# Kernel tuning notes

Measured on AMD Instinct MI355X. Metric: run time of the kernel, lower is better.

Reference implementation:

```python
import jax, jax.numpy as jnp
import numpy as np

EPS = 1e-5  # BatchNorm eps


def cbr(x, W, g, b, m, v):
    # 1x1 Conv (no bias) + inference BatchNorm + ReLU
    # x: [B,Cin,H,W], W: [Cout,Cin]
    y = jnp.einsum('oc,bchw->bohw', W, x)
    inv = g / jnp.sqrt(v + EPS)            # [Cout]
    y = y * inv[None, :, None, None] + (b - m * inv)[None, :, None, None]
    return jax.nn.relu(y)


def setup_inputs() -> dict:
    key = jax.random.key(0)
    ks = jax.random.split(key, 32)
    B, C, R, H, W = 4, 2048, 512, 64, 64
    d = {"feature": jax.random.normal(ks[0], (B, C, H, W), jnp.float32)}
    idx = 1
    for name, (cin, cout) in [("r", (C, R)), ("q", (R, R)), ("k", (R, R)), ("v", (R, R)), ("u", (R, C))]:
        d[name + "_W"] = jax.random.normal(ks[idx], (cout, cin), jnp.float32) * 0.02
        d[name + "_g"] = jax.random.uniform(ks[idx + 1], (cout,), jnp.float32)
        d[name + "_b"] = jax.random.normal(ks[idx + 2], (cout,), jnp.float32) * 0.1
        d[name + "_m"] = jax.random.normal(ks[idx + 3], (cout,), jnp.float32) * 0.1
        d[name + "_v"] = jax.random.uniform(ks[idx + 4], (cout,), jnp.float32)
        idx += 5
    return d


def reference(feature, r_W, r_g, r_b, r_m, r_v,
              q_W, q_g, q_b, q_m, q_v,
              k_W, k_g, k_b, k_m, k_v,
              v_W, v_g, v_b, v_m, v_v,
              u_W, u_g, u_b, u_m, u_v):
    B, C, H, W = feature.shape
    f = cbr(feature, r_W, r_g, r_b, r_m, r_v)          # [B,R,H,W]
    R = f.shape[1]
    N = H * W
    q = cbr(f, q_W, q_g, q_b, q_m, q_v).reshape(B, R, N)
    k = cbr(f, k_W, k_g, k_b, k_m, k_v).reshape(B, R, N)
    v = cbr(f, v_W, v_g, v_b, v_m, v_v).reshape(B, R, N)
    # similarity map over all spatial positions: [B,N,N]
    attn = jax.nn.softmax(jnp.einsum('bcn,bcm->bnm', q, k), axis=-1)
    upd = jnp.einsum('bnm,bcm->bnc', attn, v)          # [B,N,R]
    upd = upd.reshape(B, H, W, R).transpose(0, 3, 1, 2)  # [B,R,H,W]
    return cbr(f + upd, u_W, u_g, u_b, u_m, u_v)       # [B,C,H,W]
```

## Files before the change

kernel.cpp:

```cpp
#include <hip/hip_runtime.h>

#define EPSV 1e-5f

typedef unsigned short u16;
typedef __attribute__((ext_vector_type(8))) _Float16 half8;
typedef __attribute__((ext_vector_type(4))) float floatx4;

__device__ __forceinline__ float h2f(u16 h) {
    return (float)__builtin_bit_cast(_Float16, h);
}
__device__ __forceinline__ u16 f2h(float f) {
    _Float16 h = (_Float16)f;
    return __builtin_bit_cast(u16, h);
}

template <int MODE, typename OUTT>
__global__ __launch_bounds__(256)
void gemm_nt(const u16* __restrict__ A, const u16* __restrict__ B,
             OUTT* __restrict__ C_,
             const float* __restrict__ inv_, const float* __restrict__ beta_,
             const u16* __restrict__ addf,
             int K, int ldA, int ldB, int ldC,
             long strideA, long strideB, long strideC)
{
    __shared__ u16 As[128 * 32];
    __shared__ u16 Bs[128 * 32];

    const int tid = threadIdx.x;
    const int w = tid >> 6;
    const int l = tid & 63;
    const int j0 = blockIdx.x * 128;
    const int i0 = blockIdx.y * 128;

    const u16* Ab = A + (long)blockIdx.z * strideA;
    const u16* Bb = B + (long)blockIdx.z * strideB;

    const int srow = w * 16 + (l >> 2);
    const int skel = (l & 3) * 8;

    const int i_base = (w >> 1) * 64;
    const int j_base = (w & 1) * 64;
    const int lm = l & 15;
    const int kq = l >> 4;

    floatx4 acc[4][4];
    #pragma unroll
    for (int a = 0; a < 4; ++a)
        #pragma unroll
        for (int b = 0; b < 4; ++b) acc[a][b] = (floatx4)(0.0f);

    for (int k0 = 0; k0 < K; k0 += 32) {
        const u16* ga0 = Ab + (long)(i0 + srow) * ldA + k0 + skel;
        const u16* ga1 = Ab + (long)(i0 + 64 + srow) * ldA + k0 + skel;
        const u16* gb0 = Bb + (long)(j0 + srow) * ldB + k0 + skel;
        const u16* gb1 = Bb + (long)(j0 + 64 + srow) * ldB + k0 + skel;
        char* la0 = (char*)As + w * 1024;
        char* la1 = (char*)As + 4096 + w * 1024;
        char* lb0 = (char*)Bs + w * 1024;
        char* lb1 = (char*)Bs + 4096 + w * 1024;
        __builtin_amdgcn_global_load_lds(
            (const __attribute__((address_space(1))) unsigned int*)(const void*)ga0,
            (__attribute__((address_space(3))) unsigned int*)(void*)la0, 16, 0, 0);
        __builtin_amdgcn_global_load_lds(
            (const __attribute__((address_space(1))) unsigned int*)(const void*)ga1,
            (__attribute__((address_space(3))) unsigned int*)(void*)la1, 16, 0, 0);
        __builtin_amdgcn_global_load_lds(
            (const __attribute__((address_space(1))) unsigned int*)(const void*)gb0,
            (__attribute__((address_space(3))) unsigned int*)(void*)lb0, 16, 0, 0);
        __builtin_amdgcn_global_load_lds(
            (const __attribute__((address_space(1))) unsigned int*)(const void*)gb1,
            (__attribute__((address_space(3))) unsigned int*)(void*)lb1, 16, 0, 0);
        __syncthreads();

        half8 af[4], bf[4];
        #pragma unroll
        for (int t = 0; t < 4; ++t) {
            af[t] = *(const half8*)&As[(i_base + t * 16 + lm) * 32 + kq * 8];
            bf[t] = *(const half8*)&Bs[(j_base + t * 16 + lm) * 32 + kq * 8];
        }
        #pragma unroll
        for (int ti = 0; ti < 4; ++ti)
            #pragma unroll
            for (int tj = 0; tj < 4; ++tj)
                acc[ti][tj] = __builtin_amdgcn_mfma_f32_16x16x32_f16(
                    af[ti], bf[tj], acc[ti][tj], 0, 0, 0);
        __syncthreads();
    }

    OUTT* Cb = C_ + (long)blockIdx.z * strideC;
    const u16* addb = (MODE == 3) ? addf + (long)blockIdx.z * strideC : nullptr;
    #pragma unroll
    for (int ti = 0; ti < 4; ++ti) {
        #pragma unroll
        for (int tj = 0; tj < 4; ++tj) {
            const int jj = j0 + j_base + tj * 16 + lm;
            float cinv = 0.f, cbeta = 0.f;
            if (MODE == 1) { cinv = inv_[jj]; cbeta = beta_[jj]; }
            #pragma unroll
            for (int r = 0; r < 4; ++r) {
                const int ii = i0 + i_base + ti * 16 + kq * 4 + r;
                float val = acc[ti][tj][r];
                if (MODE == 1) val = fmaxf(val * cinv + cbeta, 0.0f);
                if (MODE == 2) {
                    float iv = inv_[ii], bt = beta_[ii];
                    val = fmaxf(val * iv + bt, 0.0f);
                }
                if (MODE == 3) val += h2f(addb[(long)ii * ldC + jj]);
                if (sizeof(OUTT) == 4) {
                    ((float*)Cb)[(long)ii * ldC + jj] = val;
                } else {
                    ((u16*)Cb)[(long)ii * ldC + jj] = f2h(val);
                }
            }
        }
    }
}

__global__ __launch_bounds__(256)
void conv_weight(const float* __restrict__ W, const float* __restrict__ g,
                 const float* __restrict__ b, const float* __restrict__ m,
                 const float* __restrict__ v,
                 u16* __restrict__ Wb, float* __restrict__ inv_,
                 float* __restrict__ beta_, int cout, long n)
{
    for (long idx = (long)blockIdx.x * 256 + threadIdx.x; idx < n;
         idx += (long)gridDim.x * 256)
        Wb[idx] = f2h(W[idx]);
    int c = blockIdx.x * 256 + threadIdx.x;
    if (c < cout) {
        float iv = g[c] * rsqrtf(v[c] + EPSV);
        inv_[c] = iv;
        beta_[c] = b[c] - m[c] * iv;
    }
}

__global__ __launch_bounds__(256)
void transpose_conv(const float* __restrict__ in, u16* __restrict__ out,
                    int C, int N)
{
    __shared__ float t[32][33];
    const int n0 = blockIdx.x * 32, c0 = blockIdx.y * 32;
    const float* inb = in + (long)blockIdx.z * C * N;
    u16* outb = out + (long)blockIdx.z * C * N;
    const int tx = threadIdx.x & 31, ty = threadIdx.x >> 5;
    #pragma unroll
    for (int rr = 0; rr < 32; rr += 8)
        t[ty + rr][tx] = inb[(long)(c0 + ty + rr) * N + n0 + tx];
    __syncthreads();
    #pragma unroll
    for (int rr = 0; rr < 32; rr += 8)
        outb[(long)(n0 + ty + rr) * C + c0 + tx] = f2h(t[tx][ty + rr]);
}

__global__ __launch_bounds__(256)
void softmax_f16(const float* __restrict__ S, u16* __restrict__ P)
{
    __shared__ float buf[4096];
    __shared__ float red[256];
    const float* p = S + (long)blockIdx.y * 4096 * 4096 + (long)blockIdx.x * 4096;
    u16* o = P + (long)blockIdx.y * 4096 * 4096 + (long)blockIdx.x * 4096;
    const int tid = threadIdx.x;

    float lmax = -3.4e38f;
    for (int i = tid; i < 4096; i += 256) {
        float x = p[i];
        buf[i] = x;
        lmax = fmaxf(lmax, x);
    }
    red[tid] = lmax;
    __syncthreads();
    for (int s = 128; s > 0; s >>= 1) {
        if (tid < s) red[tid] = fmaxf(red[tid], red[tid + s]);
        __syncthreads();
    }
    const float mx = red[0];
    __syncthreads();

    float lsum = 0.0f;
    for (int i = tid; i < 4096; i += 256) {
        float e = __expf(buf[i] - mx);
        buf[i] = e;
        lsum += e;
    }
    red[tid] = lsum;
    __syncthreads();
    for (int s = 128; s > 0; s >>= 1) {
        if (tid < s) red[tid] += red[tid + s];
        __syncthreads();
    }
    const float invs = 1.0f / red[0];
    __syncthreads();

    for (int i = tid; i < 4096; i += 256) o[i] = f2h(buf[i] * invs);
}

extern "C" void kernel_launch(void* const* d_in, const int* in_sizes, int n_in,
                              void* d_out, int out_size, void* d_ws, size_t ws_size,
                              hipStream_t stream)
{
    (void)in_sizes; (void)n_in; (void)out_size; (void)ws_size;
    constexpr int B = 4, C = 2048, R = 512, N = 4096;
    constexpr long NR = (long)N * R;
    constexpr long NC = (long)N * C;
    constexpr long NN = (long)N * N;

    const float* feature = (const float*)d_in[0];
    const float* W_[5]  = {(const float*)d_in[1],  (const float*)d_in[6],
                           (const float*)d_in[11], (const float*)d_in[16],
                           (const float*)d_in[21]};
    const float* G_[5]  = {(const float*)d_in[2],  (const float*)d_in[7],
                           (const float*)d_in[12], (const float*)d_in[17],
                           (const float*)d_in[22]};
    const float* Bb_[5] = {(const float*)d_in[3],  (const float*)d_in[8],
                           (const float*)d_in[13], (const float*)d_in[18],
                           (const float*)d_in[23]};
    const float* M_[5]  = {(const float*)d_in[4],  (const float*)d_in[9],
                           (const float*)d_in[14], (const float*)d_in[19],
                           (const float*)d_in[24]};
    const float* V_[5]  = {(const float*)d_in[5],  (const float*)d_in[10],
                           (const float*)d_in[15], (const float*)d_in[20],
                           (const float*)d_in[25]};
    const int cout_[5] = {R, R, R, R, C};
    const int cin_[5]  = {C, R, R, R, R};

    char* base = (char*)d_ws;
    size_t off = 0;
    float* S     = (float*)base;
    u16*   featT = (u16*)base;
    off += (size_t)B * NN * 4;
    u16* fT = (u16*)(base + off);                      off += (size_t)B * NR * 2;
    u16* qT = (u16*)(base + off);                      off += (size_t)B * NR * 2;
    u16* kT = (u16*)(base + off);                      off += (size_t)B * NR * 2;
    u16* vC = (u16*)(base + off);                      off += (size_t)B * NR * 2;
    u16* gT = (u16*)(base + off);                      off += (size_t)B * NR * 2;
    u16* Pc = (u16*)(base + off);                      off += (size_t)B * NN * 2;
    u16* Wb_[5]; float* inv_[5]; float* beta_[5];
    for (int i = 0; i < 5; ++i) {
        Wb_[i] = (u16*)(base + off);  off += (size_t)cout_[i] * cin_[i] * 2;
        off = (off + 255) & ~(size_t)255;
    }
    for (int i = 0; i < 5; ++i) {
        inv_[i]  = (float*)(base + off);  off += 8192;
        beta_[i] = (float*)(base + off);  off += 8192;
    }

    float* out = (float*)d_out;
    const dim3 blk(256);

    for (int i = 0; i < 5; ++i)
        conv_weight<<<512, blk, 0, stream>>>(W_[i], G_[i], Bb_[i], M_[i], V_[i],
                                             Wb_[i], inv_[i], beta_[i],
                                             cout_[i], (long)cout_[i] * cin_[i]);

    transpose_conv<<<dim3(N / 32, C / 32, B), blk, 0, stream>>>(feature, featT, C, N);

    gemm_nt<1, u16><<<dim3(R / 128, N / 128, B), blk, 0, stream>>>(
        featT, Wb_[0], fT, inv_[0], beta_[0], nullptr,
        C, C, C, R, NC, 0, NR);

    gemm_nt<1, u16><<<dim3(R / 128, N / 128, B), blk, 0, stream>>>(
        fT, Wb_[1], qT, inv_[1], beta_[1], nullptr,
        R, R, R, R, NR, 0, NR);
    gemm_nt<1, u16><<<dim3(R / 128, N / 128, B), blk, 0, stream>>>(
        fT, Wb_[2], kT, inv_[2], beta_[2], nullptr,
        R, R, R, R, NR, 0, NR);
    gemm_nt<2, u16><<<dim3(N / 128, R / 128, B), blk, 0, stream>>>(
        Wb_[3], fT, vC, inv_[3], beta_[3], nullptr,
        R, R, R, N, 0, NR, NR);

    gemm_nt<0, float><<<dim3(N / 128, N / 128, B), blk, 0, stream>>>(
        qT, kT, S, nullptr, nullptr, nullptr,
        R, R, R, N, NR, NR, NN);

    softmax_f16<<<dim3(N, B), blk, 0, stream>>>(S, Pc);

    gemm_nt<3, u16><<<dim3(R / 128, N / 128, B), blk, 0, stream>>>(
        Pc, vC, gT, nullptr, nullptr, fT,
        N, N, N, R, NN, NR, NR);

    gemm_nt<2, float><<<dim3(N / 128, C / 128, B), blk, 0, stream>>>(
        Wb_[4], gT, out, inv_[4], beta_[4], nullptr,
        R, R, R, N, 0, NR, NC);
}
```

Before: 828.5 us.

## Double-buffer GEMM LDS tiles, swizzle workgroup order, fuse Q/K projections

The GEMM kernel now uses two LDS buffers and issues global-to-LDS loads for the next K-slice before computing on the current one, so memory latency can overlap with MFMA work. Workgroup IDs are remapped with a stride-8 swizzle, likely to spread consecutive blocks across XCDs and improve cache locality. The Q and K projection GEMMs are merged into one GEMM with concatenated weights that writes an interleaved qk buffer, and the QK^T GEMM reads it with stride 1024. Doubling LDS per block may lower occupancy. There is also only one barrier per iteration while the next stage writes the buffer that was read in the previous iteration, which relies on that barrier for ordering.

```diff
diff --git a/kernel.cpp b/kernel.cpp
--- a/kernel.cpp
+++ b/kernel.cpp
@@ -23,17 +23,31 @@
              int K, int ldA, int ldB, int ldC,
              long strideA, long strideB, long strideC)
 {
-    __shared__ u16 As[128 * 32];
-    __shared__ u16 Bs[128 * 32];
+    __shared__ u16 As[2][128 * 32];
+    __shared__ u16 Bs[2][128 * 32];
 
     const int tid = threadIdx.x;
     const int w = tid >> 6;
     const int l = tid & 63;
-    const int j0 = blockIdx.x * 128;
-    const int i0 = blockIdx.y * 128;
-
-    const u16* Ab = A + (long)blockIdx.z * strideA;
-    const u16* Bb = B + (long)blockIdx.z * strideB;
+
+    int bx = blockIdx.x, by = blockIdx.y, bz = blockIdx.z;
+    {
+        const int gx = gridDim.x, gy = gridDim.y;
+        const int nwg = gx * gy * (int)gridDim.z;
+        if ((nwg & 7) == 0) {
+            const int lin = bx + gx * (by + gy * bz);
+            const int swz = (lin & 7) * (nwg >> 3) + (lin >> 3);
+            bx = swz % gx;
+            const int t = swz / gx;
+            by = t % gy;
+            bz = t / gy;
+        }
+    }
+    const int j0 = bx * 128;
+    const int i0 = by * 128;
+
+    const u16* Ab = A + (long)bz * strideA;
+    const u16* Bb = B + (long)bz * strideB;
 
     const int srow = w * 16 + (l >> 2);
     const int skel = (l & 3) * 8;
@@ -49,15 +63,15 @@
         #pragma unroll
         for (int b = 0; b < 4; ++b) acc[a][b] = (floatx4)(0.0f);
 
-    for (int k0 = 0; k0 < K; k0 += 32) {
+    auto stage = [&](int buf, int k0) {
         const u16* ga0 = Ab + (long)(i0 + srow) * ldA + k0 + skel;
         const u16* ga1 = Ab + (long)(i0 + 64 + srow) * ldA + k0 + skel;
         const u16* gb0 = Bb + (long)(j0 + srow) * ldB + k0 + skel;
         const u16* gb1 = Bb + (long)(j0 + 64 + srow) * ldB + k0 + skel;
-        char* la0 = (char*)As + w * 1024;
-        char* la1 = (char*)As + 4096 + w * 1024;
-        char* lb0 = (char*)Bs + w * 1024;
-        char* lb1 = (char*)Bs + 4096 + w * 1024;
+        char* la0 = (char*)&As[buf][0] + w * 1024;
+        char* la1 = (char*)&As[buf][0] + 4096 + w * 1024;
+        char* lb0 = (char*)&Bs[buf][0] + w * 1024;
+        char* lb1 = (char*)&Bs[buf][0] + 4096 + w * 1024;
         __builtin_amdgcn_global_load_lds(
             (const __attribute__((address_space(1))) unsigned int*)(const void*)ga0,
             (__attribute__((address_space(3))) unsigned int*)(void*)la0, 16, 0, 0);
@@ -70,13 +84,20 @@
         __builtin_amdgcn_global_load_lds(
             (const __attribute__((address_space(1))) unsigned int*)(const void*)gb1,
             (__attribute__((address_space(3))) unsigned int*)(void*)lb1, 16, 0, 0);
-        __syncthreads();
+    };
+
+    stage(0, 0);
+    __syncthreads();
+
+    int cur = 0;
+    for (int k0 = 0; k0 < K; k0 += 32) {
+        if (k0 + 32 < K) stage(cur ^ 1, k0 + 32);
 
         half8 af[4], bf[4];
         #pragma unroll
         for (int t = 0; t < 4; ++t) {
-            af[t] = *(const half8*)&As[(i_base + t * 16 + lm) * 32 + kq * 8];
-            bf[t] = *(const half8*)&Bs[(j_base + t * 16 + lm) * 32 + kq * 8];
+            af[t] = *(const half8*)&As[cur][(i_base + t * 16 + lm) * 32 + kq * 8];
+            bf[t] = *(const half8*)&Bs[cur][(j_base + t * 16 + lm) * 32 + kq * 8];
         }
         #pragma unroll
         for (int ti = 0; ti < 4; ++ti)
@@ -84,11 +105,13 @@
             for (int tj = 0; tj < 4; ++tj)
                 acc[ti][tj] = __builtin_amdgcn_mfma_f32_16x16x32_f16(
                     af[ti], bf[tj], acc[ti][tj], 0, 0, 0);
+
         __syncthreads();
-    }
-
-    OUTT* Cb = C_ + (long)blockIdx.z * strideC;
-    const u16* addb = (MODE == 3) ? addf + (long)blockIdx.z * strideC : nullptr;
+        cur ^= 1;
+    }
+
+    OUTT* Cb = C_ + (long)bz * strideC;
+    const u16* addb = (MODE == 3) ? addf + (long)bz * strideC : nullptr;
     #pragma unroll
     for (int ti = 0; ti < 4; ++ti) {
         #pragma unroll
@@ -203,6 +226,7 @@
     constexpr long NR = (long)N * R;
     constexpr long NC = (long)N * C;
     constexpr long NN = (long)N * N;
+    constexpr long NQK = (long)N * 1024;
 
     const float* feature = (const float*)d_in[0];
     const float* W_[5]  = {(const float*)d_in[1],  (const float*)d_in[6],
@@ -220,57 +244,63 @@
     const float* V_[5]  = {(const float*)d_in[5],  (const float*)d_in[10],
                            (const float*)d_in[15], (const float*)d_in[20],
                            (const float*)d_in[25]};
-    const int cout_[5] = {R, R, R, R, C};
-    const int cin_[5]  = {C, R, R, R, R};
 
     char* base = (char*)d_ws;
     size_t off = 0;
     float* S     = (float*)base;
     u16*   featT = (u16*)base;
     off += (size_t)B * NN * 4;
-    u16* fT = (u16*)(base + off);                      off += (size_t)B * NR * 2;
-    u16* qT = (u16*)(base + off);                      off += (size_t)B * NR * 2;
-    u16* kT = (u16*)(base + off);                      off += (size_t)B * NR * 2;
-    u16* vC = (u16*)(base + off);                      off += (size_t)B * NR * 2;
-    u16* gT = (u16*)(base + off);                      off += (size_t)B * NR * 2;
-    u16* Pc = (u16*)(base + off);                      off += (size_t)B * NN * 2;
-    u16* Wb_[5]; float* inv_[5]; float* beta_[5];
-    for (int i = 0; i < 5; ++i) {
-        Wb_[i] = (u16*)(base + off);  off += (size_t)cout_[i] * cin_[i] * 2;
-        off = (off + 255) & ~(size_t)255;
-    }
-    for (int i = 0; i < 5; ++i) {
-        inv_[i]  = (float*)(base + off);  off += 8192;
-        beta_[i] = (float*)(base + off);  off += 8192;
-    }
+    u16* fT  = (u16*)(base + off);                     off += (size_t)B * NR * 2;
+    u16* qkT = (u16*)(base + off);                     off += (size_t)B * NQK * 2;
+    u16* vC  = (u16*)(base + off);                     off += (size_t)B * NR * 2;
+    u16* gT  = (u16*)(base + off);                     off += (size_t)B * NN * 0 + (size_t)B * NR * 2;
+    u16* Pc  = (u16*)(base + off);                     off += (size_t)B * NN * 2;
+    u16* Wb_r  = (u16*)(base + off);  off += (size_t)R * C * 2;
+    u16* WbQK  = (u16*)(base + off);  off += (size_t)1024 * R * 2;
+    u16* Wb_v  = (u16*)(base + off);  off += (size_t)R * R * 2;
+    u16* Wb_u  = (u16*)(base + off);  off += (size_t)C * R * 2;
+    off = (off + 255) & ~(size_t)255;
+    float* inv_r  = (float*)(base + off);  off += 8192;
+    float* beta_r = (float*)(base + off);  off += 8192;
+    float* invQK  = (float*)(base + off);  off += 8192;
+    float* betaQK = (float*)(base + off);  off += 8192;
+    float* inv_v  = (float*)(base + off);  off += 8192;
+    float* beta_v = (float*)(base + off);  off += 8192;
+    float* inv_u  = (float*)(base + off);  off += 8192;
+    float* beta_u = (float*)(base + off);  off += 8192;
 
     float* out = (float*)d_out;
     const dim3 blk(256);
 
-    for (int i = 0; i < 5; ++i)
-        conv_weight<<<512, blk, 0, stream>>>(W_[i], G_[i], Bb_[i], M_[i], V_[i],
-                                             Wb_[i], inv_[i], beta_[i],
-                                             cout_[i], (long)cout_[i] * cin_[i]);
+    conv_weight<<<512, blk, 0, stream>>>(W_[0], G_[0], Bb_[0], M_[0], V_[0],
+                                         Wb_r, inv_r, beta_r, R, (long)R * C);
+    conv_weight<<<512, blk, 0, stream>>>(W_[1], G_[1], Bb_[1], M_[1], V_[1],
+                                         WbQK, invQK, betaQK, R, (long)R * R);
+    conv_weight<<<512, blk, 0, stream>>>(W_[2], G_[2], Bb_[2], M_[2], V_[2],
+                                         WbQK + (size_t)R * R, invQK + R, betaQK + R,
+                                         R, (long)R * R);
+    conv_weight<<<512, blk, 0, stream>>>(W_[3], G_[3], Bb_[3], M_[3], V_[3],
+                                         Wb_v, inv_v, beta_v, R, (long)R * R);
+    conv_weight<<<512, blk, 0, stream>>>(W_[4], G_[4], Bb_[4], M_[4], V_[4],
+                                         Wb_u, inv_u, beta_u, C, (long)C * R);
 
     transpose_conv<<<dim3(N / 32, C / 32, B), blk, 0, stream>>>(feature, featT, C, N);
 
     gemm_nt<1, u16><<<dim3(R / 128, N / 128, B), blk, 0, stream>>>(
-        featT, Wb_[0], fT, inv_[0], beta_[0], nullptr,
+        featT, Wb_r, fT, inv_r, beta_r, nullptr,
         C, C, C, R, NC, 0, NR);
 
-    gemm_nt<1, u16><<<dim3(R / 128, N / 128, B), blk, 0, stream>>>(
-        fT, Wb_[1], qT, inv_[1], beta_[1], nullptr,
-        R, R, R, R, NR, 0, NR);
-    gemm_nt<1, u16><<<dim3(R / 128, N / 128, B), blk, 0, stream>>>(
-        fT, Wb_[2], kT, inv_[2], beta_[2], nullptr,
-        R, R, R, R, NR, 0, NR);
+    gemm_nt<1, u16><<<dim3(1024 / 128, N / 128, B), blk, 0, stream>>>(
+        fT, WbQK, qkT, invQK, betaQK, nullptr,
+        R, R, R, 1024, NR, 0, NQK);
+
     gemm_nt<2, u16><<<dim3(N / 128, R / 128, B), blk, 0, stream>>>(
-        Wb_[3], fT, vC, inv_[3], beta_[3], nullptr,
+        Wb_v, fT, vC, inv_v, beta_v, nullptr,
         R, R, R, N, 0, NR, NR);
 
     gemm_nt<0, float><<<dim3(N / 128, N / 128, B), blk, 0, stream>>>(
-        qT, kT, S, nullptr, nullptr, nullptr,
-        R, R, R, N, NR, NR, NN);
+        qkT, qkT + 512, S, nullptr, nullptr, nullptr,
+        R, 1024, 1024, N, NQK, NQK, NN);
 
     softmax_f16<<<dim3(N, B), blk, 0, stream>>>(S, Pc);
 
@@ -279,6 +309,6 @@
         N, N, N, R, NN, NR, NR);
 
     gemm_nt<2, float><<<dim3(N / 128, C / 128, B), blk, 0, stream>>>(
-        Wb_[4], gT, out, inv_[4], beta_[4], nullptr,
+        Wb_u, gT, out, inv_u, beta_u, nullptr,
         R, R, R, N, 0, NR, NC);
 }
```

Measured after the change: 793.6 us. 1.04x faster.
